# Kernel optimization log

Measured on AMD Instinct MI355X. Metric: run time of the kernel, lower is better.

Reference implementation:

```python
import jax, jax.numpy as jnp
import numpy as np

N = 100_000      # nodes
E = 1_600_000    # edges (before self-loops)
IN = 128         # in_dim
H = 4            # heads (layer 1)
C = 32           # hidden_dim (per-head channels)
ED = 16          # edge_dim
NEG_SLOPE = 0.2  # PyG GATConv default


def setup_inputs() -> dict:
    key = jax.random.key(0)
    ks = jax.random.split(key, 16)
    s = 0.05
    return {
        "x": jax.random.normal(ks[0], (N, IN), jnp.float32),
        "edge_index": jax.random.randint(ks[1], (2, E), 0, N, dtype=jnp.int32),
        "edge_attr": jax.random.normal(ks[2], (E, ED), jnp.float32),
        # layer 1 params (heads=H, concat=True)
        "W1": jax.random.normal(ks[3], (IN, H * C), jnp.float32) * s,
        "W1e": jax.random.normal(ks[4], (ED, H * C), jnp.float32) * s,
        "a1_src": jax.random.normal(ks[5], (H, C), jnp.float32) * s,
        "a1_dst": jax.random.normal(ks[6], (H, C), jnp.float32) * s,
        "a1_edge": jax.random.normal(ks[7], (H, C), jnp.float32) * s,
        "b1": jax.random.normal(ks[8], (H * C,), jnp.float32) * s,
        # layer 2 params (heads=1, concat=False)
        "W2": jax.random.normal(ks[9], (H * C, C), jnp.float32) * s,
        "W2e": jax.random.normal(ks[10], (ED, C), jnp.float32) * s,
        "a2_src": jax.random.normal(ks[11], (1, C), jnp.float32) * s,
        "a2_dst": jax.random.normal(ks[12], (1, C), jnp.float32) * s,
        "a2_edge": jax.random.normal(ks[13], (1, C), jnp.float32) * s,
        "b2": jax.random.normal(ks[14], (C,), jnp.float32) * s,
    }


def _add_self_loops(src, dst, edge_attr, n):
    # PyG GATConv: add_self_loops=True, fill_value='mean' -> self-loop edge_attr
    # is the mean of incoming edge attrs per target node.
    deg = jax.ops.segment_sum(jnp.ones_like(dst, jnp.float32), dst, num_segments=n)
    mean_attr = jax.ops.segment_sum(edge_attr, dst, num_segments=n) / jnp.maximum(deg, 1.0)[:, None]
    loop = jnp.arange(n, dtype=src.dtype)
    src2 = jnp.concatenate([src, loop])
    dst2 = jnp.concatenate([dst, loop])
    attr2 = jnp.concatenate([edge_attr, mean_attr], axis=0)
    return src2, dst2, attr2


def _gat_conv(x, src, dst, eattr, W, We, a_s, a_d, a_e, b, concat):
    n = x.shape[0]
    Hh, Cc = a_s.shape
    h = (x @ W).reshape(n, Hh, Cc)                # [N,H,C]
    he = (eattr @ We).reshape(-1, Hh, Cc)          # [E',H,C]
    al_s = jnp.sum(h * a_s, axis=-1)               # [N,H]
    al_d = jnp.sum(h * a_d, axis=-1)               # [N,H]
    al_e = jnp.sum(he * a_e, axis=-1)              # [E',H]
    e = jax.nn.leaky_relu(al_s[src] + al_d[dst] + al_e, NEG_SLOPE)  # [E',H]
    # segment softmax over destination node neighborhoods
    m = jax.ops.segment_max(e, dst, num_segments=n)                 # [N,H]
    p = jnp.exp(e - m[dst])
    z = jax.ops.segment_sum(p, dst, num_segments=n)                 # [N,H]
    alpha = p / z[dst]                                              # [E',H]
    out = jax.ops.segment_sum(alpha[:, :, None] * h[src], dst, num_segments=n)  # [N,H,C]
    if concat:
        out = out.reshape(n, Hh * Cc)
    else:
        out = out.mean(axis=1)
    return out + b, alpha


def reference(x, edge_index, edge_attr,
              W1, W1e, a1_src, a1_dst, a1_edge, b1,
              W2, W2e, a2_src, a2_dst, a2_edge, b2):
    n = x.shape[0]
    src, dst, eattr = _add_self_loops(edge_index[0], edge_index[1], edge_attr, n)
    h1, _ = _gat_conv(x, src, dst, eattr, W1, W1e, a1_src, a1_dst, a1_edge, b1, concat=True)
    h1 = jax.nn.elu(h1)
    # dropout p applied in training only; inference reference -> identity
    h2, alpha2 = _gat_conv(h1, src, dst, eattr, W2, W2e, a2_src, a2_dst, a2_edge, b2, concat=False)
    h2 = jax.nn.elu(h2)
    edge_index_sl = jnp.stack([src, dst])
    return h2, edge_index_sl, alpha2
```

## Files before the change

kernel.cpp:

```cpp
#include <hip/hip_runtime.h>

#define NN 100000
#define NE 1600000
#define NE2 1700000
#define OUT_EI 3200000
#define OUT_AL 6600000
#define SLOPE 0.2f
#define NB 391
#define EPB 6400
#define NBB 250

typedef unsigned short u16;
typedef unsigned int u32;
typedef __bf16 bf16x8 __attribute__((ext_vector_type(8)));
typedef float f32x4 __attribute__((ext_vector_type(4)));
typedef u32 u32x4 __attribute__((ext_vector_type(4)));

__device__ __forceinline__ float bf2f(u16 u){ return __uint_as_float(((u32)u) << 16); }
__device__ __forceinline__ u16 f2bf(float f){
    u32 x = __float_as_uint(f);
    x += 0x7FFFu + ((x >> 16) & 1u);
    return (u16)(x >> 16);
}
__device__ __forceinline__ float eluf(float v){ return v > 0.f ? v : (__expf(v) - 1.f); }
__device__ __forceinline__ float lreluf(float v){ return fmaxf(v, SLOPE * v); }

__global__ __launch_bounds__(256) void k_bhist(const int* __restrict__ ei, int* __restrict__ bcnt){
    __shared__ int s[NB];
    int t = threadIdx.x;
    for (int i = t; i < NB; i += 256) s[i] = 0;
    __syncthreads();
    int e0 = blockIdx.x * EPB;
    for (int i = t; i < EPB; i += 256)
        atomicAdd(&s[ei[NE + e0 + i] >> 8], 1);
    __syncthreads();
    for (int i = t; i < NB; i += 256) if (s[i]) atomicAdd(&bcnt[i], s[i]);
}

__global__ void k_bscan(const int* __restrict__ bcnt, int* __restrict__ bbase, int* __restrict__ bcur){
    __shared__ int s[512];
    int t = threadIdx.x;
    int v = (t < NB) ? bcnt[t] : 0;
    s[t] = v; __syncthreads();
    #pragma unroll
    for (int d = 1; d < 512; d <<= 1){
        int x = (t >= d) ? s[t - d] : 0;
        __syncthreads();
        s[t] += x;
        __syncthreads();
    }
    if (t < NB){ int ex = s[t] - v; bbase[t] = ex; bcur[t] = ex; }
    if (t == 0) bbase[NB] = NE;
}

__global__ __launch_bounds__(256) void k_bscatter(const int* __restrict__ ei, const u16* __restrict__ ale1,
                                                  const u16* __restrict__ ale2,
                                                  int* __restrict__ bcur, int4* __restrict__ bins,
                                                  u16* __restrict__ binsA2){
    __shared__ int cnt[NB];
    __shared__ int base[NB];
    int t = threadIdx.x;
    for (int i = t; i < NB; i += 256) cnt[i] = 0;
    __syncthreads();
    int e0 = blockIdx.x * EPB;
    for (int i = t; i < EPB; i += 256)
        atomicAdd(&cnt[ei[NE + e0 + i] >> 8], 1);
    __syncthreads();
    for (int i = t; i < NB; i += 256){
        int c = cnt[i];
        base[i] = c ? atomicAdd(&bcur[i], c) : 0;
        cnt[i] = 0;
    }
    __syncthreads();
    const u32* a1 = (const u32*)ale1;
    for (int i = t; i < EPB; i += 256){
        int e = e0 + i;
        int dst = ei[NE + e];
        int b = dst >> 8;
        int r = atomicAdd(&cnt[b], 1);
        int pos = base[b] + r;
        int4 v;
        v.x = ei[e];
        v.y = dst;
        v.z = (int)a1[2 * e];
        v.w = (int)a1[2 * e + 1];
        bins[pos] = v;
        binsA2[pos] = ale2[e];
    }
}

__global__ __launch_bounds__(256) void k_bdeg(const int4* __restrict__ bins, const int* __restrict__ bbase,
                                              int* __restrict__ deg){
    __shared__ int d[256];
    int t = threadIdx.x, b = blockIdx.x;
    d[t] = 0;
    __syncthreads();
    int s = bbase[b], e2 = bbase[b + 1];
    const int* bd = (const int*)bins;
    for (int i = s + t; i < e2; i += 256)
        atomicAdd(&d[bd[(size_t)i * 4 + 1] & 255], 1);
    __syncthreads();
    int n = b * 256 + t;
    if (n < NN) deg[n] = d[t];
}

__global__ __launch_bounds__(256) void k_scan_blk(const int* __restrict__ deg, int* __restrict__ part,
                                                  int* __restrict__ bsum){
    __shared__ int s[256];
    int t = threadIdx.x;
    int i = blockIdx.x * 256 + t;
    int v = (i < NN) ? deg[i] : 0;
    s[t] = v; __syncthreads();
    #pragma unroll
    for (int d = 1; d < 256; d <<= 1){
        int x = (t >= d) ? s[t - d] : 0;
        __syncthreads();
        s[t] += x;
        __syncthreads();
    }
    if (i < NN) part[i] = s[t] - v;
    if (t == 255) bsum[blockIdx.x] = s[255];
}

__global__ void k_scan_top(int* __restrict__ bsum){
    __shared__ int s[512];
    int t = threadIdx.x;
    int v = (t < NB) ? bsum[t] : 0;
    s[t] = v; __syncthreads();
    #pragma unroll
    for (int d = 1; d < 512; d <<= 1){
        int x = (t >= d) ? s[t - d] : 0;
        __syncthreads();
        s[t] += x;
        __syncthreads();
    }
    bsum[t] = s[t] - v;
}

__global__ __launch_bounds__(256) void k_scan_add(const int* __restrict__ part, const int* __restrict__ bsum,
                                                  int* __restrict__ offsets){
    int i = blockIdx.x * 256 + threadIdx.x;
    if (i >= NN) return;
    offsets[i] = part[i] + bsum[i >> 8] + i;
    if (i == 0) offsets[NN] = NE + NN;
}

__global__ __launch_bounds__(256) void k_fscatter(const int4* __restrict__ bins, const u16* __restrict__ binsA2,
                                                  const int* __restrict__ bbase, const int* __restrict__ offsets,
                                                  int* __restrict__ src32, ushort4* __restrict__ ale1p,
                                                  u16* __restrict__ ale2p){
    __shared__ int cur[256];
    int t = threadIdx.x, b = blockIdx.x;
    int n = b * 256 + t;
    if (n < NN) cur[t] = offsets[n] + 1;
    __syncthreads();
    int s = bbase[b], e2 = bbase[b + 1];
    for (int i = s + t; i < e2; i += 256){
        int4 v = bins[i];
        int pos = atomicAdd(&cur[v.y & 255], 1);
        src32[pos] = v.x;
        uint2 a; a.x = (u32)v.z; a.y = (u32)v.w;
        ((uint2*)ale1p)[pos] = a;
        ale2p[pos] = binsA2[i];
    }
}

__global__ void k_q(const float* __restrict__ W1e, const float* __restrict__ a1e,
                    const float* __restrict__ W2e, const float* __restrict__ a2e,
                    float* __restrict__ q1, float* __restrict__ q2){
    int t = threadIdx.x;
    int k = t >> 2, h = t & 3;
    float s = 0.f;
    for (int c = 0; c < 32; c++) s += W1e[k * 128 + h * 32 + c] * a1e[h * 32 + c];
    q1[t] = s;
    if (t < 16){
        float s2 = 0.f;
        for (int c = 0; c < 32; c++) s2 += W2e[t * 32 + c] * a2e[c];
        q2[t] = s2;
    }
}

__global__ __launch_bounds__(256) void k_ale(const float* __restrict__ eattr,
                                             const float* __restrict__ q1, const float* __restrict__ q2,
                                             u16* __restrict__ ale1, u16* __restrict__ ale2){
    __shared__ float sq1[64], sq2[16];
    int t = threadIdx.x;
    if (t < 64) sq1[t] = q1[t];
    if (t < 16) sq2[t] = q2[t];
    __syncthreads();
    int gt = blockIdx.x * 256 + t;
    int e = gt >> 2, part = gt & 3;
    f32x4 av = ((const f32x4*)eattr)[(size_t)e * 4 + part];
    int j0 = part * 4;
    float p0 = 0, p1 = 0, p2 = 0, p3 = 0, p4 = 0;
    #pragma unroll
    for (int k = 0; k < 4; k++){
        float a = av[k]; int j = j0 + k;
        p0 += a * sq1[j * 4 + 0]; p1 += a * sq1[j * 4 + 1];
        p2 += a * sq1[j * 4 + 2]; p3 += a * sq1[j * 4 + 3];
        p4 += a * sq2[j];
    }
    #pragma unroll
    for (int m = 1; m < 4; m <<= 1){
        p0 += __shfl_xor(p0, m); p1 += __shfl_xor(p1, m);
        p2 += __shfl_xor(p2, m); p3 += __shfl_xor(p3, m); p4 += __shfl_xor(p4, m);
    }
    if (part == 0){
        ushort4 w; w.x = f2bf(p0); w.y = f2bf(p1); w.z = f2bf(p2); w.w = f2bf(p3);
        ((ushort4*)ale1)[e] = w;
        ale2[e] = f2bf(p4);
    }
}

__global__ __launch_bounds__(256) void k_gemm1(const float* __restrict__ x, const float* __restrict__ W,
                                               u16* __restrict__ h1){
    __shared__ __align__(16) u16 sW[128 * 136];
    int t = threadIdx.x;
    for (int i = t; i < 128 * 128; i += 256){
        int k = i >> 7, c = i & 127;
        sW[c * 136 + k] = f2bf(W[i]);
    }
    __syncthreads();
    int lane = t & 63, wave = t >> 6;
    int quad = lane >> 4, m16 = lane & 15;
    int rowA = blockIdx.x * 64 + wave * 16 + m16;
    bf16x8 afr[4];
    if (rowA < NN){
        const f32x4* xr = (const f32x4*)(x + (size_t)rowA * 128);
        #pragma unroll
        for (int kk = 0; kk < 4; kk++){
            f32x4 va = xr[kk * 8 + quad * 2];
            f32x4 vb = xr[kk * 8 + quad * 2 + 1];
            #pragma unroll
            for (int i = 0; i < 4; i++){ afr[kk][i] = (__bf16)va[i]; afr[kk][4 + i] = (__bf16)vb[i]; }
        }
    } else {
        #pragma unroll
        for (int kk = 0; kk < 4; kk++)
            #pragma unroll
            for (int i = 0; i < 8; i++) afr[kk][i] = (__bf16)0.f;
    }
    int rowbase = blockIdx.x * 64 + wave * 16 + quad * 4;
    #pragma unroll
    for (int nt = 0; nt < 8; nt++){
        f32x4 acc = (f32x4){0.f, 0.f, 0.f, 0.f};
        const u16* wp = &sW[(nt * 16 + m16) * 136 + quad * 8];
        #pragma unroll
        for (int kk = 0; kk < 4; kk++){
            bf16x8 bfr = *(const bf16x8*)(wp + kk * 32);
            acc = __builtin_amdgcn_mfma_f32_16x16x32_bf16(afr[kk], bfr, acc, 0, 0, 0);
        }
        int col = nt * 16 + m16;
        #pragma unroll
        for (int r = 0; r < 4; r++){
            int row = rowbase + r;
            if (row < NN) h1[(size_t)row * 128 + col] = f2bf(acc[r]);
        }
    }
}

__global__ __launch_bounds__(256) void k_gemm2(const u16* __restrict__ hin, const float* __restrict__ W,
                                               float* __restrict__ h2a){
    __shared__ __align__(16) u16 sW[32 * 136];
    int t = threadIdx.x;
    for (int i = t; i < 128 * 32; i += 256){
        int k = i >> 5, c = i & 31;
        sW[c * 136 + k] = f2bf(W[i]);
    }
    __syncthreads();
    int lane = t & 63, wave = t >> 6;
    int quad = lane >> 4, m16 = lane & 15;
    int rowA = blockIdx.x * 64 + wave * 16 + m16;
    bf16x8 afr[4];
    if (rowA < NN){
        const u16* xr = hin + (size_t)rowA * 128 + quad * 8;
        #pragma unroll
        for (int kk = 0; kk < 4; kk++) afr[kk] = *(const bf16x8*)(xr + kk * 32);
    } else {
        #pragma unroll
        for (int kk = 0; kk < 4; kk++)
            #pragma unroll
            for (int i = 0; i < 8; i++) afr[kk][i] = (__bf16)0.f;
    }
    int rowbase = blockIdx.x * 64 + wave * 16 + quad * 4;
    #pragma unroll
    for (int nt = 0; nt < 2; nt++){
        f32x4 acc = (f32x4){0.f, 0.f, 0.f, 0.f};
        const u16* wp = &sW[(nt * 16 + m16) * 136 + quad * 8];
        #pragma unroll
        for (int kk = 0; kk < 4; kk++){
            bf16x8 bfr = *(const bf16x8*)(wp + kk * 32);
            acc = __builtin_amdgcn_mfma_f32_16x16x32_bf16(afr[kk], bfr, acc, 0, 0, 0);
        }
        int col = nt * 16 + m16;
        #pragma unroll
        for (int r = 0; r < 4; r++){
            int row = rowbase + r;
            if (row < NN) h2a[(size_t)row * 32 + col] = acc[r];
        }
    }
}

__global__ __launch_bounds__(256) void k_al1(const u16* __restrict__ h1, const float* __restrict__ a1s,
                                             const float* __restrict__ a1d,
                                             float* __restrict__ al_s, float* __restrict__ al_d){
    int idx = blockIdx.x * 256 + threadIdx.x;
    int j = idx & 127;
    float v = bf2f(h1[idx]);
    float vs = v * a1s[j];
    float vd = v * a1d[j];
    #pragma unroll
    for (int m = 1; m < 32; m <<= 1){ vs += __shfl_xor(vs, m); vd += __shfl_xor(vd, m); }
    if ((threadIdx.x & 31) == 0){
        int n = idx >> 7, h = j >> 5;
        al_s[n * 4 + h] = vs;
        al_d[n * 4 + h] = vd;
    }
}

__global__ __launch_bounds__(256) void k_al2(const float* __restrict__ h2a, const float* __restrict__ a2s,
                                             const float* __restrict__ a2d,
                                             float* __restrict__ al_s, float* __restrict__ al_d){
    int idx = blockIdx.x * 256 + threadIdx.x;
    int c = idx & 31;
    float v = h2a[idx];
    float vs = v * a2s[c];
    float vd = v * a2d[c];
    #pragma unroll
    for (int m = 1; m < 32; m <<= 1){ vs += __shfl_xor(vs, m); vd += __shfl_xor(vd, m); }
    if ((threadIdx.x & 31) == 0){
        int n = idx >> 5;
        al_s[n] = vs;
        al_d[n] = vd;
    }
}

__global__ __launch_bounds__(256) void k_node1(const int* __restrict__ src32, const ushort4* __restrict__ ale1p,
                                               const int* __restrict__ offsets,
                                               const float* __restrict__ al_s, const float* __restrict__ al_d,
                                               const u16* __restrict__ h1, const float* __restrict__ b1,
                                               u16* __restrict__ h1b, ushort4* __restrict__ pb1){
    int wave = threadIdx.x >> 6, lane = threadIdx.x & 63;
    int n = blockIdx.x * 4 + wave;
    int start = offsets[n], end = offsets[n + 1];
    int degr = end - start - 1;
    f32x4 ald  = ((const f32x4*)al_d)[n];
    f32x4 alsn = ((const f32x4*)al_s)[n];
    float z0 = 0, z1 = 0, z2 = 0, z3 = 0, s0 = 0, s1 = 0, s2 = 0, s3 = 0;
    for (int i = start + 1 + lane; i < end; i += 64){
        int src = src32[i];
        ushort4 av = ale1p[i];
        f32x4 als = ((const f32x4*)al_s)[src];
        float a0 = bf2f(av.x), a1 = bf2f(av.y), a2 = bf2f(av.z), a3 = bf2f(av.w);
        float e0 = __expf(lreluf(als[0] + ald[0] + a0));
        float e1 = __expf(lreluf(als[1] + ald[1] + a1));
        float e2 = __expf(lreluf(als[2] + ald[2] + a2));
        float e3 = __expf(lreluf(als[3] + ald[3] + a3));
        z0 += e0; z1 += e1; z2 += e2; z3 += e3;
        s0 += a0; s1 += a1; s2 += a2; s3 += a3;
        ushort4 w; w.x = f2bf(e0); w.y = f2bf(e1); w.z = f2bf(e2); w.w = f2bf(e3);
        pb1[i] = w;
    }
    #pragma unroll
    for (int m = 1; m < 64; m <<= 1){
        z0 += __shfl_xor(z0, m); z1 += __shfl_xor(z1, m); z2 += __shfl_xor(z2, m); z3 += __shfl_xor(z3, m);
        s0 += __shfl_xor(s0, m); s1 += __shfl_xor(s1, m); s2 += __shfl_xor(s2, m); s3 += __shfl_xor(s3, m);
    }
    float inv_deg = 1.f / fmaxf((float)degr, 1.f);
    float p0 = __expf(lreluf(alsn[0] + ald[0] + s0 * inv_deg)); z0 += p0;
    float p1 = __expf(lreluf(alsn[1] + ald[1] + s1 * inv_deg)); z1 += p1;
    float p2 = __expf(lreluf(alsn[2] + ald[2] + s2 * inv_deg)); z2 += p2;
    float p3 = __expf(lreluf(alsn[3] + ald[3] + s3 * inv_deg)); z3 += p3;
    int g = lane >> 4, l = lane & 15, hq = l >> 2;
    float rz = 1.f / ((hq == 0) ? z0 : (hq == 1) ? z1 : (hq == 2) ? z2 : z3);
    float ps = (hq == 0) ? p0 : (hq == 1) ? p1 : (hq == 2) ? p2 : p3;
    const u32x4* h1v = (const u32x4*)h1;
    const u16* pbu = (const u16*)pb1;
    float acc[8];
    #pragma unroll
    for (int k = 0; k < 8; k++) acc[k] = 0.f;
    for (int i = start + g; i < end; i += 4){
        bool slf = (i == start);
        int src = slf ? n : src32[i];
        float p = slf ? ps : bf2f(pbu[(size_t)i * 4 + hq]);
        u32x4 v = h1v[(size_t)src * 16 + l];
        #pragma unroll
        for (int k = 0; k < 4; k++){
            acc[2 * k]     += p * bf2f((u16)(v[k] & 0xFFFFu));
            acc[2 * k + 1] += p * bf2f((u16)(v[k] >> 16));
        }
    }
    #pragma unroll
    for (int k = 0; k < 8; k++){
        acc[k] += __shfl_xor(acc[k], 16);
        acc[k] += __shfl_xor(acc[k], 32);
    }
    if (g == 0){
        u32x4 w;
        #pragma unroll
        for (int k = 0; k < 4; k++){
            float v0 = eluf(acc[2 * k]     * rz + b1[l * 8 + 2 * k]);
            float v1 = eluf(acc[2 * k + 1] * rz + b1[l * 8 + 2 * k + 1]);
            w[k] = (u32)f2bf(v0) | ((u32)f2bf(v1) << 16);
        }
        ((u32x4*)h1b)[(size_t)n * 16 + l] = w;
    }
}

__global__ __launch_bounds__(256) void k_node2(const int* __restrict__ src32, const u16* __restrict__ ale2p,
                                               const int* __restrict__ offsets,
                                               const float* __restrict__ al_s, const float* __restrict__ al_d,
                                               const float* __restrict__ h2a, const float* __restrict__ b2,
                                               float* __restrict__ dout, u16* __restrict__ pb2,
                                               float* __restrict__ rzv){
    int wave = threadIdx.x >> 6, lane = threadIdx.x & 63;
    int n = blockIdx.x * 4 + wave;
    int start = offsets[n], end = offsets[n + 1];
    int degr = end - start - 1;
    float aldn = al_d[n];
    float z = 0.f, sa = 0.f;
    for (int i = start + 1 + lane; i < end; i += 64){
        int src = src32[i];
        float a = bf2f(ale2p[i]);
        float ev = __expf(lreluf(al_s[src] + aldn + a));
        z += ev; sa += a;
        pb2[i] = f2bf(ev);
    }
    #pragma unroll
    for (int m = 1; m < 64; m <<= 1){ z += __shfl_xor(z, m); sa += __shfl_xor(sa, m); }
    float mal = sa / fmaxf((float)degr, 1.f);
    float pself = __expf(lreluf(al_s[n] + aldn + mal));
    z += pself;
    float rz = 1.f / z;
    if (lane == 0){
        rzv[n] = rz;
        dout[OUT_AL + NE + n] = pself * rz;
    }
    int g = lane >> 3, l = lane & 7;
    const f32x4* h2v = (const f32x4*)h2a;
    f32x4 acc = (f32x4){0.f, 0.f, 0.f, 0.f};
    for (int i = start + g; i < end; i += 8){
        bool slf = (i == start);
        int src = slf ? n : src32[i];
        float alpha = (slf ? pself : bf2f(pb2[i])) * rz;
        f32x4 v = h2v[(size_t)src * 8 + l];
        #pragma unroll
        for (int k = 0; k < 4; k++) acc[k] += alpha * v[k];
    }
    #pragma unroll
    for (int k = 0; k < 4; k++){
        acc[k] += __shfl_xor(acc[k], 8);
        acc[k] += __shfl_xor(acc[k], 16);
        acc[k] += __shfl_xor(acc[k], 32);
    }
    if (g == 0){
        f32x4 w;
        #pragma unroll
        for (int k = 0; k < 4; k++) w[k] = eluf(acc[k] + b2[l * 4 + k]);
        ((f32x4*)dout)[(size_t)n * 8 + l] = w;
    }
}

__global__ __launch_bounds__(256) void k_alpha(const int* __restrict__ ei, const u16* __restrict__ ale2,
                                               const float* __restrict__ al_s, const float* __restrict__ al_d,
                                               const float* __restrict__ rzv, float* __restrict__ dout){
    int e = blockIdx.x * 256 + threadIdx.x;
    int src = ei[e], dst = ei[NE + e];
    float a = bf2f(ale2[e]);
    float ev = __expf(lreluf(al_s[src] + al_d[dst] + a));
    dout[OUT_AL + e] = ev * rzv[dst];
}

__global__ __launch_bounds__(256) void k_eidx(const int* __restrict__ ei, float* __restrict__ dout){
    int i = blockIdx.x * 256 + threadIdx.x;
    if (i >= 2 * NE2) return;
    int val;
    if (i < NE2) val = (i < NE) ? ei[i] : (i - NE);
    else { int e = i - NE2; val = (e < NE) ? ei[NE + e] : (e - NE); }
    dout[OUT_EI + i] = (float)val;
}

extern "C" void kernel_launch(void* const* d_in, const int* in_sizes, int n_in,
                              void* d_out, int out_size, void* d_ws, size_t ws_size,
                              hipStream_t stream) {
    const float* x     = (const float*)d_in[0];
    const int*   ei    = (const int*)d_in[1];
    const float* eattr = (const float*)d_in[2];
    const float* W1    = (const float*)d_in[3];
    const float* W1e   = (const float*)d_in[4];
    const float* a1s   = (const float*)d_in[5];
    const float* a1d   = (const float*)d_in[6];
    const float* a1e   = (const float*)d_in[7];
    const float* b1    = (const float*)d_in[8];
    const float* W2    = (const float*)d_in[9];
    const float* W2e   = (const float*)d_in[10];
    const float* a2s   = (const float*)d_in[11];
    const float* a2d   = (const float*)d_in[12];
    const float* a2e   = (const float*)d_in[13];
    const float* b2    = (const float*)d_in[14];
    float* dout = (float*)d_out;

    char* ws = (char*)d_ws;
    size_t off = 0;
    auto alloc = [&](size_t bytes) -> void* {
        void* p = ws + off;
        off += (bytes + 255) & ~(size_t)255;
        return p;
    };
    int* bcnt = (int*)alloc((size_t)NB * 4);
    size_t zero_bytes = off;
    int*     deg     = (int*)alloc((size_t)NN * 4);
    int*     part    = (int*)alloc((size_t)NN * 4);
    int*     bsum    = (int*)alloc(512 * 4);
    int*     offsets = (int*)alloc((size_t)(NN + 1) * 4);
    int*     bbase   = (int*)alloc((size_t)(NB + 1) * 4);
    int*     bcur    = (int*)alloc((size_t)NB * 4);
    int4*    bins    = (int4*)alloc((size_t)NE * 16);
    u16*     binsA2  = (u16*)alloc((size_t)NE * 2);
    int*     src32   = (int*)alloc((size_t)NE2 * 4);
    ushort4* ale1p   = (ushort4*)alloc((size_t)NE2 * 8);
    u16*     ale2p   = (u16*)alloc((size_t)NE2 * 2);
    float*   q1      = (float*)alloc(64 * 4);
    float*   q2      = (float*)alloc(16 * 4);
    u16*     ale1    = (u16*)alloc((size_t)NE * 4 * 2);
    u16*     ale2    = (u16*)alloc((size_t)NE * 2);
    float*   al_s1   = (float*)alloc((size_t)NN * 4 * 4);
    float*   al_d1   = (float*)alloc((size_t)NN * 4 * 4);
    u16*     h1      = (u16*)alloc((size_t)NN * 128 * 2);
    u16*     h1b     = (u16*)alloc((size_t)NN * 128 * 2);
    ushort4* pb1   = (ushort4*)bins;
    u16*   pb2   = (u16*)ale1;
    char*  h1r   = (char*)h1;
    float* h2a   = (float*)(h1r);
    float* al_s2 = (float*)(h1r + 12800000);
    float* al_d2 = (float*)(h1r + 13200128);
    float* rzv   = (float*)(h1r + 13600256);

    const int TB = 256;
    hipMemsetAsync(d_ws, 0, zero_bytes, stream);

    k_q<<<1, 64, 0, stream>>>(W1e, a1e, W2e, a2e, q1, q2);
    k_ale<<<NE * 4 / TB, TB, 0, stream>>>(eattr, q1, q2, ale1, ale2);
    k_bhist<<<NBB, TB, 0, stream>>>(ei, bcnt);
    k_bscan<<<1, 512, 0, stream>>>(bcnt, bbase, bcur);
    k_bscatter<<<NBB, TB, 0, stream>>>(ei, ale1, ale2, bcur, bins, binsA2);
    k_bdeg<<<NB, TB, 0, stream>>>(bins, bbase, deg);
    k_scan_blk<<<NB, TB, 0, stream>>>(deg, part, bsum);
    k_scan_top<<<1, 512, 0, stream>>>(bsum);
    k_scan_add<<<NB, TB, 0, stream>>>(part, bsum, offsets);
    k_fscatter<<<NB, TB, 0, stream>>>(bins, binsA2, bbase, offsets, src32, ale1p, ale2p);
    k_gemm1<<<(NN + 63) / 64, TB, 0, stream>>>(x, W1, h1);
    k_al1<<<NN * 128 / TB, TB, 0, stream>>>(h1, a1s, a1d, al_s1, al_d1);
    k_node1<<<NN / 4, TB, 0, stream>>>(src32, ale1p, offsets, al_s1, al_d1, h1, b1, h1b, pb1);
    k_gemm2<<<(NN + 63) / 64, TB, 0, stream>>>(h1b, W2, h2a);
    k_al2<<<NN * 32 / TB, TB, 0, stream>>>(h2a, a2s, a2d, al_s2, al_d2);
    k_node2<<<NN / 4, TB, 0, stream>>>(src32, ale2p, offsets, al_s2, al_d2, h2a, b2, dout, pb2, rzv);
    k_alpha<<<NE / TB, TB, 0, stream>>>(ei, ale2, al_s2, al_d2, rzv, dout);
    k_eidx<<<(2 * NE2 + TB - 1) / TB, TB, 0, stream>>>(ei, dout);
}
```

Before: 589.2 us.

## Fuse CSR build, attention logits into GEMMs, and single-pass node aggregation

Compacts the binned edge record into a packed 32-bit src+local-dst word plus a separate attribute array. Degree counting, the prefix scan and the final scatter are merged into one per-bin kernel, since bins align with 256-node blocks. Attention dot products are fused into the MFMA GEMM epilogues, and both node kernels become single-pass: unnormalised exp weights are accumulated alongside the feature sums and divided by z at the end, which removes the pb1/pb2 buffers. Edge-index output writes are folded into k_alpha and k_node2, and several kernel launches disappear. No max-subtraction is used in the softmax, and the packed src field limits node ids to 24 bits.

```diff
diff --git a/kernel.cpp b/kernel.cpp
--- a/kernel.cpp
+++ b/kernel.cpp
@@ -24,6 +24,11 @@
 }
 __device__ __forceinline__ float eluf(float v){ return v > 0.f ? v : (__expf(v) - 1.f); }
 __device__ __forceinline__ float lreluf(float v){ return fmaxf(v, SLOPE * v); }
+__device__ __forceinline__ float sel4f(float a, float b, float c, float d, int s){
+    float x = (s & 1) ? b : a;
+    float y = (s & 1) ? d : c;
+    return (s & 2) ? y : x;
+}
 
 __global__ __launch_bounds__(256) void k_bhist(const int* __restrict__ ei, int* __restrict__ bcnt){
     __shared__ int s[NB];
@@ -55,16 +60,20 @@
 
 __global__ __launch_bounds__(256) void k_bscatter(const int* __restrict__ ei, const u16* __restrict__ ale1,
                                                   const u16* __restrict__ ale2,
-                                                  int* __restrict__ bcur, int4* __restrict__ bins,
-                                                  u16* __restrict__ binsA2){
+                                                  int* __restrict__ bcur, u32* __restrict__ binsP,
+                                                  uint2* __restrict__ binsA, u16* __restrict__ binsA2){
     __shared__ int cnt[NB];
     __shared__ int base[NB];
+    __shared__ int sdst[EPB];
     int t = threadIdx.x;
     for (int i = t; i < NB; i += 256) cnt[i] = 0;
     __syncthreads();
     int e0 = blockIdx.x * EPB;
-    for (int i = t; i < EPB; i += 256)
-        atomicAdd(&cnt[ei[NE + e0 + i] >> 8], 1);
+    for (int i = t; i < EPB; i += 256){
+        int dv = ei[NE + e0 + i];
+        sdst[i] = dv;
+        atomicAdd(&cnt[dv >> 8], 1);
+    }
     __syncthreads();
     for (int i = t; i < NB; i += 256){
         int c = cnt[i];
@@ -72,95 +81,55 @@
         cnt[i] = 0;
     }
     __syncthreads();
-    const u32* a1 = (const u32*)ale1;
+    const uint2* a1 = (const uint2*)ale1;
     for (int i = t; i < EPB; i += 256){
         int e = e0 + i;
-        int dst = ei[NE + e];
+        int dst = sdst[i];
         int b = dst >> 8;
         int r = atomicAdd(&cnt[b], 1);
         int pos = base[b] + r;
-        int4 v;
-        v.x = ei[e];
-        v.y = dst;
-        v.z = (int)a1[2 * e];
-        v.w = (int)a1[2 * e + 1];
-        bins[pos] = v;
+        binsP[pos] = ((u32)(dst & 255) << 24) | (u32)ei[e];
+        binsA[pos] = a1[e];
         binsA2[pos] = ale2[e];
     }
 }
 
-__global__ __launch_bounds__(256) void k_bdeg(const int4* __restrict__ bins, const int* __restrict__ bbase,
-                                              int* __restrict__ deg){
+__global__ __launch_bounds__(256) void k_fscatter(const u32* __restrict__ binsP, const uint2* __restrict__ binsA,
+                                                  const u16* __restrict__ binsA2, const int* __restrict__ bbase,
+                                                  int* __restrict__ offsets,
+                                                  int* __restrict__ src32, uint2* __restrict__ ale1p,
+                                                  u16* __restrict__ ale2p){
     __shared__ int d[256];
+    __shared__ int s[256];
+    __shared__ int cur[256];
     int t = threadIdx.x, b = blockIdx.x;
     d[t] = 0;
     __syncthreads();
-    int s = bbase[b], e2 = bbase[b + 1];
-    const int* bd = (const int*)bins;
-    for (int i = s + t; i < e2; i += 256)
-        atomicAdd(&d[bd[(size_t)i * 4 + 1] & 255], 1);
-    __syncthreads();
-    int n = b * 256 + t;
-    if (n < NN) deg[n] = d[t];
-}
-
-__global__ __launch_bounds__(256) void k_scan_blk(const int* __restrict__ deg, int* __restrict__ part,
-                                                  int* __restrict__ bsum){
-    __shared__ int s[256];
-    int t = threadIdx.x;
-    int i = blockIdx.x * 256 + t;
-    int v = (i < NN) ? deg[i] : 0;
+    int bs = bbase[b], be = bbase[b + 1];
+    for (int i = bs + t; i < be; i += 256)
+        atomicAdd(&d[binsP[i] >> 24], 1);
+    __syncthreads();
+    int v = d[t];
     s[t] = v; __syncthreads();
     #pragma unroll
-    for (int d = 1; d < 256; d <<= 1){
-        int x = (t >= d) ? s[t - d] : 0;
+    for (int dd = 1; dd < 256; dd <<= 1){
+        int x = (t >= dd) ? s[t - dd] : 0;
         __syncthreads();
         s[t] += x;
         __syncthreads();
     }
-    if (i < NN) part[i] = s[t] - v;
-    if (t == 255) bsum[blockIdx.x] = s[255];
-}
-
-__global__ void k_scan_top(int* __restrict__ bsum){
-    __shared__ int s[512];
-    int t = threadIdx.x;
-    int v = (t < NB) ? bsum[t] : 0;
-    s[t] = v; __syncthreads();
-    #pragma unroll
-    for (int d = 1; d < 512; d <<= 1){
-        int x = (t >= d) ? s[t - d] : 0;
-        __syncthreads();
-        s[t] += x;
-        __syncthreads();
-    }
-    bsum[t] = s[t] - v;
-}
-
-__global__ __launch_bounds__(256) void k_scan_add(const int* __restrict__ part, const int* __restrict__ bsum,
-                                                  int* __restrict__ offsets){
-    int i = blockIdx.x * 256 + threadIdx.x;
-    if (i >= NN) return;
-    offsets[i] = part[i] + bsum[i >> 8] + i;
-    if (i == 0) offsets[NN] = NE + NN;
-}
-
-__global__ __launch_bounds__(256) void k_fscatter(const int4* __restrict__ bins, const u16* __restrict__ binsA2,
-                                                  const int* __restrict__ bbase, const int* __restrict__ offsets,
-                                                  int* __restrict__ src32, ushort4* __restrict__ ale1p,
-                                                  u16* __restrict__ ale2p){
-    __shared__ int cur[256];
-    int t = threadIdx.x, b = blockIdx.x;
     int n = b * 256 + t;
-    if (n < NN) cur[t] = offsets[n] + 1;
-    __syncthreads();
-    int s = bbase[b], e2 = bbase[b + 1];
-    for (int i = s + t; i < e2; i += 256){
-        int4 v = bins[i];
-        int pos = atomicAdd(&cur[v.y & 255], 1);
-        src32[pos] = v.x;
-        uint2 a; a.x = (u32)v.z; a.y = (u32)v.w;
-        ((uint2*)ale1p)[pos] = a;
+    int off = bs + (s[t] - v) + n;
+    if (n < NN) offsets[n] = off;
+    cur[t] = off + 1;
+    if (b == 0 && t == 0) offsets[NN] = NE + NN;
+    __syncthreads();
+    for (int i = bs + t; i < be; i += 256){
+        u32 p = binsP[i];
+        int dl = p >> 24;
+        int pos = atomicAdd(&cur[dl], 1);
+        src32[pos] = (int)(p & 0xFFFFFFu);
+        ale1p[pos] = binsA[i];
         ale2p[pos] = binsA2[i];
     }
 }
@@ -213,7 +182,9 @@
 }
 
 __global__ __launch_bounds__(256) void k_gemm1(const float* __restrict__ x, const float* __restrict__ W,
-                                               u16* __restrict__ h1){
+                                               const float* __restrict__ a1s, const float* __restrict__ a1d,
+                                               u16* __restrict__ h1,
+                                               float* __restrict__ al_s, float* __restrict__ al_d){
     __shared__ __align__(16) u16 sW[128 * 136];
     int t = threadIdx.x;
     for (int i = t; i < 128 * 128; i += 256){
@@ -232,15 +203,20 @@
             f32x4 va = xr[kk * 8 + quad * 2];
             f32x4 vb = xr[kk * 8 + quad * 2 + 1];
             #pragma unroll
-            for (int i = 0; i < 4; i++){ afr[kk][i] = (__bf16)va[i]; afr[kk][4 + i] = (__bf16)vb[i]; }
+            for (int i2 = 0; i2 < 4; i2++){ afr[kk][i2] = (__bf16)va[i2]; afr[kk][4 + i2] = (__bf16)vb[i2]; }
         }
     } else {
         #pragma unroll
         for (int kk = 0; kk < 4; kk++)
             #pragma unroll
-            for (int i = 0; i < 8; i++) afr[kk][i] = (__bf16)0.f;
+            for (int i2 = 0; i2 < 8; i2++) afr[kk][i2] = (__bf16)0.f;
     }
     int rowbase = blockIdx.x * 64 + wave * 16 + quad * 4;
+    float vsA[4][4], vdA[4][4];
+    #pragma unroll
+    for (int r = 0; r < 4; r++)
+        #pragma unroll
+        for (int h = 0; h < 4; h++){ vsA[r][h] = 0.f; vdA[r][h] = 0.f; }
     #pragma unroll
     for (int nt = 0; nt < 8; nt++){
         f32x4 acc = (f32x4){0.f, 0.f, 0.f, 0.f};
@@ -251,16 +227,47 @@
             acc = __builtin_amdgcn_mfma_f32_16x16x32_bf16(afr[kk], bfr, acc, 0, 0, 0);
         }
         int col = nt * 16 + m16;
+        float cs = a1s[col], cd = a1d[col];
+        const int h = nt >> 1;
         #pragma unroll
         for (int r = 0; r < 4; r++){
+            vsA[r][h] += acc[r] * cs;
+            vdA[r][h] += acc[r] * cd;
             int row = rowbase + r;
             if (row < NN) h1[(size_t)row * 128 + col] = f2bf(acc[r]);
         }
     }
+    #pragma unroll
+    for (int r = 0; r < 4; r++)
+        #pragma unroll
+        for (int h = 0; h < 4; h++)
+            #pragma unroll
+            for (int m = 1; m < 16; m <<= 1){
+                vsA[r][h] += __shfl_xor(vsA[r][h], m);
+                vdA[r][h] += __shfl_xor(vdA[r][h], m);
+            }
+    int rs = m16 >> 2, hs = m16 & 3;
+    float s0 = sel4f(vsA[0][0], vsA[0][1], vsA[0][2], vsA[0][3], hs);
+    float s1 = sel4f(vsA[1][0], vsA[1][1], vsA[1][2], vsA[1][3], hs);
+    float s2 = sel4f(vsA[2][0], vsA[2][1], vsA[2][2], vsA[2][3], hs);
+    float s3 = sel4f(vsA[3][0], vsA[3][1], vsA[3][2], vsA[3][3], hs);
+    float d0 = sel4f(vdA[0][0], vdA[0][1], vdA[0][2], vdA[0][3], hs);
+    float d1 = sel4f(vdA[1][0], vdA[1][1], vdA[1][2], vdA[1][3], hs);
+    float d2 = sel4f(vdA[2][0], vdA[2][1], vdA[2][2], vdA[2][3], hs);
+    float d3 = sel4f(vdA[3][0], vdA[3][1], vdA[3][2], vdA[3][3], hs);
+    float souts = sel4f(s0, s1, s2, s3, rs);
+    float soutd = sel4f(d0, d1, d2, d3, rs);
+    int row = rowbase + rs;
+    if (row < NN){
+        al_s[row * 4 + hs] = souts;
+        al_d[row * 4 + hs] = soutd;
+    }
 }
 
 __global__ __launch_bounds__(256) void k_gemm2(const u16* __restrict__ hin, const float* __restrict__ W,
-                                               float* __restrict__ h2a){
+                                               const float* __restrict__ a2s, const float* __restrict__ a2d,
+                                               float* __restrict__ h2a,
+                                               float* __restrict__ al_s, float* __restrict__ al_d){
     __shared__ __align__(16) u16 sW[32 * 136];
     int t = threadIdx.x;
     for (int i = t; i < 128 * 32; i += 256){
@@ -280,9 +287,12 @@
         #pragma unroll
         for (int kk = 0; kk < 4; kk++)
             #pragma unroll
-            for (int i = 0; i < 8; i++) afr[kk][i] = (__bf16)0.f;
+            for (int i2 = 0; i2 < 8; i2++) afr[kk][i2] = (__bf16)0.f;
     }
     int rowbase = blockIdx.x * 64 + wave * 16 + quad * 4;
+    float vs2[4], vd2[4];
+    #pragma unroll
+    for (int r = 0; r < 4; r++){ vs2[r] = 0.f; vd2[r] = 0.f; }
     #pragma unroll
     for (int nt = 0; nt < 2; nt++){
         f32x4 acc = (f32x4){0.f, 0.f, 0.f, 0.f};
@@ -293,101 +303,75 @@
             acc = __builtin_amdgcn_mfma_f32_16x16x32_bf16(afr[kk], bfr, acc, 0, 0, 0);
         }
         int col = nt * 16 + m16;
+        float cs = a2s[col], cd = a2d[col];
         #pragma unroll
         for (int r = 0; r < 4; r++){
+            vs2[r] += acc[r] * cs;
+            vd2[r] += acc[r] * cd;
             int row = rowbase + r;
             if (row < NN) h2a[(size_t)row * 32 + col] = acc[r];
         }
     }
-}
-
-__global__ __launch_bounds__(256) void k_al1(const u16* __restrict__ h1, const float* __restrict__ a1s,
-                                             const float* __restrict__ a1d,
-                                             float* __restrict__ al_s, float* __restrict__ al_d){
-    int idx = blockIdx.x * 256 + threadIdx.x;
-    int j = idx & 127;
-    float v = bf2f(h1[idx]);
-    float vs = v * a1s[j];
-    float vd = v * a1d[j];
-    #pragma unroll
-    for (int m = 1; m < 32; m <<= 1){ vs += __shfl_xor(vs, m); vd += __shfl_xor(vd, m); }
-    if ((threadIdx.x & 31) == 0){
-        int n = idx >> 7, h = j >> 5;
-        al_s[n * 4 + h] = vs;
-        al_d[n * 4 + h] = vd;
-    }
-}
-
-__global__ __launch_bounds__(256) void k_al2(const float* __restrict__ h2a, const float* __restrict__ a2s,
-                                             const float* __restrict__ a2d,
-                                             float* __restrict__ al_s, float* __restrict__ al_d){
-    int idx = blockIdx.x * 256 + threadIdx.x;
-    int c = idx & 31;
-    float v = h2a[idx];
-    float vs = v * a2s[c];
-    float vd = v * a2d[c];
-    #pragma unroll
-    for (int m = 1; m < 32; m <<= 1){ vs += __shfl_xor(vs, m); vd += __shfl_xor(vd, m); }
-    if ((threadIdx.x & 31) == 0){
-        int n = idx >> 5;
-        al_s[n] = vs;
-        al_d[n] = vd;
-    }
-}
-
-__global__ __launch_bounds__(256) void k_node1(const int* __restrict__ src32, const ushort4* __restrict__ ale1p,
+    #pragma unroll
+    for (int r = 0; r < 4; r++)
+        #pragma unroll
+        for (int m = 1; m < 16; m <<= 1){
+            vs2[r] += __shfl_xor(vs2[r], m);
+            vd2[r] += __shfl_xor(vd2[r], m);
+        }
+    if (m16 < 4){
+        int row = rowbase + m16;
+        if (row < NN){
+            al_s[row] = sel4f(vs2[0], vs2[1], vs2[2], vs2[3], m16);
+            al_d[row] = sel4f(vd2[0], vd2[1], vd2[2], vd2[3], m16);
+        }
+    }
+}
+
+__global__ __launch_bounds__(256) void k_node1(const int* __restrict__ src32, const u16* __restrict__ ale1u,
                                                const int* __restrict__ offsets,
                                                const float* __restrict__ al_s, const float* __restrict__ al_d,
                                                const u16* __restrict__ h1, const float* __restrict__ b1,
-                                               u16* __restrict__ h1b, ushort4* __restrict__ pb1){
+                                               u16* __restrict__ h1b){
     int wave = threadIdx.x >> 6, lane = threadIdx.x & 63;
     int n = blockIdx.x * 4 + wave;
     int start = offsets[n], end = offsets[n + 1];
     int degr = end - start - 1;
-    f32x4 ald  = ((const f32x4*)al_d)[n];
-    f32x4 alsn = ((const f32x4*)al_s)[n];
-    float z0 = 0, z1 = 0, z2 = 0, z3 = 0, s0 = 0, s1 = 0, s2 = 0, s3 = 0;
-    for (int i = start + 1 + lane; i < end; i += 64){
-        int src = src32[i];
-        ushort4 av = ale1p[i];
-        f32x4 als = ((const f32x4*)al_s)[src];
-        float a0 = bf2f(av.x), a1 = bf2f(av.y), a2 = bf2f(av.z), a3 = bf2f(av.w);
-        float e0 = __expf(lreluf(als[0] + ald[0] + a0));
-        float e1 = __expf(lreluf(als[1] + ald[1] + a1));
-        float e2 = __expf(lreluf(als[2] + ald[2] + a2));
-        float e3 = __expf(lreluf(als[3] + ald[3] + a3));
-        z0 += e0; z1 += e1; z2 += e2; z3 += e3;
-        s0 += a0; s1 += a1; s2 += a2; s3 += a3;
-        ushort4 w; w.x = f2bf(e0); w.y = f2bf(e1); w.z = f2bf(e2); w.w = f2bf(e3);
-        pb1[i] = w;
-    }
-    #pragma unroll
-    for (int m = 1; m < 64; m <<= 1){
-        z0 += __shfl_xor(z0, m); z1 += __shfl_xor(z1, m); z2 += __shfl_xor(z2, m); z3 += __shfl_xor(z3, m);
-        s0 += __shfl_xor(s0, m); s1 += __shfl_xor(s1, m); s2 += __shfl_xor(s2, m); s3 += __shfl_xor(s3, m);
-    }
+    int g = lane >> 4, l = lane & 15, hq = l >> 2;
+    float aldh = al_d[n * 4 + hq];
+    const u32x4* h1v = (const u32x4*)h1;
+    float acc[8];
+    #pragma unroll
+    for (int k = 0; k < 8; k++) acc[k] = 0.f;
+    float z = 0.f, sa = 0.f;
+    int i = start + 1 + g;
+    int src = (i < end) ? __builtin_nontemporal_load(src32 + i) : 0;
+    for (; i < end; i += 4){
+        int ni = i + 4;
+        int nsrc = (ni < end) ? __builtin_nontemporal_load(src32 + ni) : 0;
+        float a = bf2f(__builtin_nontemporal_load(ale1u + (size_t)i * 4 + hq));
+        float als = al_s[src * 4 + hq];
+        u32x4 v = h1v[(size_t)src * 16 + l];
+        float e = __expf(lreluf(als + aldh + a));
+        z += e; sa += a;
+        #pragma unroll
+        for (int k = 0; k < 4; k++){
+            acc[2 * k]     += e * bf2f((u16)(v[k] & 0xFFFFu));
+            acc[2 * k + 1] += e * bf2f((u16)(v[k] >> 16));
+        }
+        src = nsrc;
+    }
+    z += __shfl_xor(z, 16); z += __shfl_xor(z, 32);
+    sa += __shfl_xor(sa, 16); sa += __shfl_xor(sa, 32);
     float inv_deg = 1.f / fmaxf((float)degr, 1.f);
-    float p0 = __expf(lreluf(alsn[0] + ald[0] + s0 * inv_deg)); z0 += p0;
-    float p1 = __expf(lreluf(alsn[1] + ald[1] + s1 * inv_deg)); z1 += p1;
-    float p2 = __expf(lreluf(alsn[2] + ald[2] + s2 * inv_deg)); z2 += p2;
-    float p3 = __expf(lreluf(alsn[3] + ald[3] + s3 * inv_deg)); z3 += p3;
-    int g = lane >> 4, l = lane & 15, hq = l >> 2;
-    float rz = 1.f / ((hq == 0) ? z0 : (hq == 1) ? z1 : (hq == 2) ? z2 : z3);
-    float ps = (hq == 0) ? p0 : (hq == 1) ? p1 : (hq == 2) ? p2 : p3;
-    const u32x4* h1v = (const u32x4*)h1;
-    const u16* pbu = (const u16*)pb1;
-    float acc[8];
-    #pragma unroll
-    for (int k = 0; k < 8; k++) acc[k] = 0.f;
-    for (int i = start + g; i < end; i += 4){
-        bool slf = (i == start);
-        int src = slf ? n : src32[i];
-        float p = slf ? ps : bf2f(pbu[(size_t)i * 4 + hq]);
-        u32x4 v = h1v[(size_t)src * 16 + l];
+    float ps = __expf(lreluf(al_s[n * 4 + hq] + aldh + sa * inv_deg));
+    z += ps;
+    if (g == 0){
+        u32x4 v = h1v[(size_t)n * 16 + l];
         #pragma unroll
         for (int k = 0; k < 4; k++){
-            acc[2 * k]     += p * bf2f((u16)(v[k] & 0xFFFFu));
-            acc[2 * k + 1] += p * bf2f((u16)(v[k] >> 16));
+            acc[2 * k]     += ps * bf2f((u16)(v[k] & 0xFFFFu));
+            acc[2 * k + 1] += ps * bf2f((u16)(v[k] >> 16));
         }
     }
     #pragma unroll
@@ -396,6 +380,7 @@
         acc[k] += __shfl_xor(acc[k], 32);
     }
     if (g == 0){
+        float rz = 1.f / z;
         u32x4 w;
         #pragma unroll
         for (int k = 0; k < 4; k++){
@@ -411,41 +396,46 @@
                                                const int* __restrict__ offsets,
                                                const float* __restrict__ al_s, const float* __restrict__ al_d,
                                                const float* __restrict__ h2a, const float* __restrict__ b2,
-                                               float* __restrict__ dout, u16* __restrict__ pb2,
-                                               float* __restrict__ rzv){
+                                               float* __restrict__ dout, float* __restrict__ rzv){
     int wave = threadIdx.x >> 6, lane = threadIdx.x & 63;
     int n = blockIdx.x * 4 + wave;
     int start = offsets[n], end = offsets[n + 1];
     int degr = end - start - 1;
     float aldn = al_d[n];
-    float z = 0.f, sa = 0.f;
-    for (int i = start + 1 + lane; i < end; i += 64){
-        int src = src32[i];
-        float a = bf2f(ale2p[i]);
-        float ev = __expf(lreluf(al_s[src] + aldn + a));
-        z += ev; sa += a;
-        pb2[i] = f2bf(ev);
-    }
-    #pragma unroll
-    for (int m = 1; m < 64; m <<= 1){ z += __shfl_xor(z, m); sa += __shfl_xor(sa, m); }
-    float mal = sa / fmaxf((float)degr, 1.f);
-    float pself = __expf(lreluf(al_s[n] + aldn + mal));
-    z += pself;
-    float rz = 1.f / z;
-    if (lane == 0){
-        rzv[n] = rz;
-        dout[OUT_AL + NE + n] = pself * rz;
-    }
     int g = lane >> 3, l = lane & 7;
     const f32x4* h2v = (const f32x4*)h2a;
     f32x4 acc = (f32x4){0.f, 0.f, 0.f, 0.f};
-    for (int i = start + g; i < end; i += 8){
-        bool slf = (i == start);
-        int src = slf ? n : src32[i];
-        float alpha = (slf ? pself : bf2f(pb2[i])) * rz;
+    float z = 0.f, sa = 0.f;
+    int i = start + 1 + g;
+    int src = (i < end) ? __builtin_nontemporal_load(src32 + i) : 0;
+    for (; i < end; i += 8){
+        int ni = i + 8;
+        int nsrc = (ni < end) ? __builtin_nontemporal_load(src32 + ni) : 0;
+        float a = bf2f(__builtin_nontemporal_load(ale2p + i));
+        float als = al_s[src];
         f32x4 v = h2v[(size_t)src * 8 + l];
-        #pragma unroll
-        for (int k = 0; k < 4; k++) acc[k] += alpha * v[k];
+        float e = __expf(lreluf(als + aldn + a));
+        z += e; sa += a;
+        #pragma unroll
+        for (int k = 0; k < 4; k++) acc[k] += e * v[k];
+        src = nsrc;
+    }
+    z += __shfl_xor(z, 8); z += __shfl_xor(z, 16); z += __shfl_xor(z, 32);
+    sa += __shfl_xor(sa, 8); sa += __shfl_xor(sa, 16); sa += __shfl_xor(sa, 32);
+    float mal = sa / fmaxf((float)degr, 1.f);
+    float ps = __expf(lreluf(al_s[n] + aldn + mal));
+    z += ps;
+    float rz = 1.f / z;
+    if (g == 0){
+        f32x4 v = h2v[(size_t)n * 8 + l];
+        #pragma unroll
+        for (int k = 0; k < 4; k++) acc[k] += ps * v[k];
+    }
+    if (lane == 0){
+        rzv[n] = rz;
+        dout[OUT_AL + NE + n] = ps * rz;
+        dout[OUT_EI + NE + n] = (float)n;
+        dout[OUT_EI + NE2 + NE + n] = (float)n;
     }
     #pragma unroll
     for (int k = 0; k < 4; k++){
@@ -468,16 +458,9 @@
     int src = ei[e], dst = ei[NE + e];
     float a = bf2f(ale2[e]);
     float ev = __expf(lreluf(al_s[src] + al_d[dst] + a));
-    dout[OUT_AL + e] = ev * rzv[dst];
-}
-
-__global__ __launch_bounds__(256) void k_eidx(const int* __restrict__ ei, float* __restrict__ dout){
-    int i = blockIdx.x * 256 + threadIdx.x;
-    if (i >= 2 * NE2) return;
-    int val;
-    if (i < NE2) val = (i < NE) ? ei[i] : (i - NE);
-    else { int e = i - NE2; val = (e < NE) ? ei[NE + e] : (e - NE); }
-    dout[OUT_EI + i] = (float)val;
+    __builtin_nontemporal_store(ev * rzv[dst], &dout[OUT_AL + e]);
+    __builtin_nontemporal_store((float)src, &dout[OUT_EI + e]);
+    __builtin_nontemporal_store((float)dst, &dout[OUT_EI + NE2 + e]);
 }
 
 extern "C" void kernel_launch(void* const* d_in, const int* in_sizes, int n_in,
@@ -509,16 +492,14 @@
     };
     int* bcnt = (int*)alloc((size_t)NB * 4);
     size_t zero_bytes = off;
-    int*     deg     = (int*)alloc((size_t)NN * 4);
-    int*     part    = (int*)alloc((size_t)NN * 4);
-    int*     bsum    = (int*)alloc(512 * 4);
     int*     offsets = (int*)alloc((size_t)(NN + 1) * 4);
     int*     bbase   = (int*)alloc((size_t)(NB + 1) * 4);
     int*     bcur    = (int*)alloc((size_t)NB * 4);
-    int4*    bins    = (int4*)alloc((size_t)NE * 16);
+    u32*     binsP   = (u32*)alloc((size_t)NE * 4);
+    uint2*   binsA   = (uint2*)alloc((size_t)NE * 8);
     u16*     binsA2  = (u16*)alloc((size_t)NE * 2);
     int*     src32   = (int*)alloc((size_t)NE2 * 4);
-    ushort4* ale1p   = (ushort4*)alloc((size_t)NE2 * 8);
+    uint2*   ale1p   = (uint2*)alloc((size_t)NE2 * 8);
     u16*     ale2p   = (u16*)alloc((size_t)NE2 * 2);
     float*   q1      = (float*)alloc(64 * 4);
     float*   q2      = (float*)alloc(16 * 4);
@@ -528,8 +509,6 @@
     float*   al_d1   = (float*)alloc((size_t)NN * 4 * 4);
     u16*     h1      = (u16*)alloc((size_t)NN * 128 * 2);
     u16*     h1b     = (u16*)alloc((size_t)NN * 128 * 2);
-    ushort4* pb1   = (ushort4*)bins;
-    u16*   pb2   = (u16*)ale1;
     char*  h1r   = (char*)h1;
     float* h2a   = (float*)(h1r);
     float* al_s2 = (float*)(h1r + 12800000);
@@ -543,18 +522,11 @@
     k_ale<<<NE * 4 / TB, TB, 0, stream>>>(eattr, q1, q2, ale1, ale2);
     k_bhist<<<NBB, TB, 0, stream>>>(ei, bcnt);
     k_bscan<<<1, 512, 0, stream>>>(bcnt, bbase, bcur);
-    k_bscatter<<<NBB, TB, 0, stream>>>(ei, ale1, ale2, bcur, bins, binsA2);
-    k_bdeg<<<NB, TB, 0, stream>>>(bins, bbase, deg);
-    k_scan_blk<<<NB, TB, 0, stream>>>(deg, part, bsum);
-    k_scan_top<<<1, 512, 0, stream>>>(bsum);
-    k_scan_add<<<NB, TB, 0, stream>>>(part, bsum, offsets);
-    k_fscatter<<<NB, TB, 0, stream>>>(bins, binsA2, bbase, offsets, src32, ale1p, ale2p);
-    k_gemm1<<<(NN + 63) / 64, TB, 0, stream>>>(x, W1, h1);
-    k_al1<<<NN * 128 / TB, TB, 0, stream>>>(h1, a1s, a1d, al_s1, al_d1);
-    k_node1<<<NN / 4, TB, 0, stream>>>(src32, ale1p, offsets, al_s1, al_d1, h1, b1, h1b, pb1);
-    k_gemm2<<<(NN + 63) / 64, TB, 0, stream>>>(h1b, W2, h2a);
-    k_al2<<<NN * 32 / TB, TB, 0, stream>>>(h2a, a2s, a2d, al_s2, al_d2);
-    k_node2<<<NN / 4, TB, 0, stream>>>(src32, ale2p, offsets, al_s2, al_d2, h2a, b2, dout, pb2, rzv);
+    k_bscatter<<<NBB, TB, 0, stream>>>(ei, ale1, ale2, bcur, binsP, binsA, binsA2);
+    k_fscatter<<<NB, TB, 0, stream>>>(binsP, binsA, binsA2, bbase, offsets, src32, ale1p, ale2p);
+    k_gemm1<<<(NN + 63) / 64, TB, 0, stream>>>(x, W1, a1s, a1d, h1, al_s1, al_d1);
+    k_node1<<<NN / 4, TB, 0, stream>>>(src32, (const u16*)ale1p, offsets, al_s1, al_d1, h1, b1, h1b);
+    k_gemm2<<<(NN + 63) / 64, TB, 0, stream>>>(h1b, W2, a2s, a2d, h2a, al_s2, al_d2);
+    k_node2<<<NN / 4, TB, 0, stream>>>(src32, ale2p, offsets, al_s2, al_d2, h2a, b2, dout, rzv);
     k_alpha<<<NE / TB, TB, 0, stream>>>(ei, ale2, al_s2, al_d2, rzv, dout);
-    k_eidx<<<(2 * NE2 + TB - 1) / TB, TB, 0, stream>>>(ei, dout);
-}
+}
```

Measured after the change: 562.1 us. -4.6%, faster.
